# Kernel tuning notes

Measured on AMD Instinct MI355X. Metric: run time of the kernel, lower is better.

## Reference

```python
import jax, jax.numpy as jnp
import numpy as np

N, K, F_IN, F_OUT, P = 50000, 32, 64, 64, 3


def setup_inputs() -> dict:
    key = jax.random.key(0)
    k1, k2, k3, k4, k5 = jax.random.split(key, 5)
    h = jax.random.normal(k1, (N, F_IN), dtype=jnp.float32)
    pos = jax.random.normal(k2, (N, P), dtype=jnp.float32)
    neighbor_idx = jax.random.randint(k3, (N, K), 0, N, dtype=jnp.int32)
    weight = jax.random.normal(k4, (K * F_IN, F_OUT), dtype=jnp.float32) * 0.02
    bias_p = jax.random.normal(k5, (1, F_OUT), dtype=jnp.float32) * 0.02
    return {"h": h, "pos": pos, "neighbor_idx": neighbor_idx,
            "weight": weight, "bias_p": bias_p}


def reference(h, pos, neighbor_idx, weight, bias_p):
    n, k = neighbor_idx.shape
    msgs = h[neighbor_idx]                      # [N, K, F_IN] gather
    diff = pos[:, None, :] - pos[neighbor_idx]  # [N, K, P]
    sq = jnp.sum(diff * diff, axis=2, keepdims=True)  # [N, K, 1]
    # torch: dist[dist==0] = 0.5 ; safe-sqrt avoids NaN grads at 0
    dist = jnp.where(sq == 0.0, 0.5, jnp.sqrt(jnp.where(sq == 0.0, 1.0, sq)))
    wow = (msgs / dist).reshape(n, k * h.shape[1])  # [N, K*F_IN]
    h1 = wow @ weight + bias_p                   # [N, F_OUT]
    return jax.nn.leaky_relu(h1, negative_slope=0.01)
```

## Files before the change

### kernel.cpp

```cpp
#include <hip/hip_runtime.h>


#define N_NODES 50000
#define KN      32
#define FIN     64
#define FOUT    64
#define MTILE   64

typedef __attribute__((ext_vector_type(4))) float    f32x4;
typedef __attribute__((ext_vector_type(8))) _Float16 f16x8;

static __device__ __forceinline__ f16x8 dec8i(unsigned int x, unsigned int y) {
    union { unsigned int w[4]; f16x8 v; } r;
    unsigned int xh = x >> 16, yh = y >> 16;
    r.w[0] = 0x64006400u | ((x  & 0xFFu) << 2) | ((x  & 0xFF00u) << 10);
    r.w[1] = 0x64006400u | ((xh & 0xFFu) << 2) | ((xh & 0xFF00u) << 10);
    r.w[2] = 0x64006400u | ((y  & 0xFFu) << 2) | ((y  & 0xFF00u) << 10);
    r.w[3] = 0x64006400u | ((yh & 0xFFu) << 2) | ((yh & 0xFF00u) << 10);
    return r.v;
}

__global__ void k_prep(const float* __restrict__ w, _Float16* __restrict__ wf,
                       const float* __restrict__ h, unsigned char* __restrict__ hq,
                       const float* __restrict__ pos, float4* __restrict__ posx) {
    __shared__ float s_w[64 * 64];
    const int tid = threadIdx.x;
    if (blockIdx.x < 32) {
        const int kn = blockIdx.x;
        for (int p = tid; p < 64 * 64; p += 256)
            s_w[p] = w[kn * 64 * 64 + p];
        __syncthreads();
        const int t = tid >> 6, lane = tid & 63;
        const int lm = lane & 15, q = lane >> 4;
        #pragma unroll
        for (int jh = 0; jh < 2; ++jh) {
            f16x8 o;
            #pragma unroll
            for (int i = 0; i < 8; ++i)
                o[i] = (_Float16)s_w[(q * 16 + jh * 8 + i) * 64 + t * 16 + lm];
            *(f16x8*)(wf + ((kn * 2 + jh) * 4 + t) * 512 + lane * 8) = o;
        }
    } else {
        const int r = (blockIdx.x - 32) * 256 + tid;
        if (r < N_NODES) {
            const float* hr = h + (size_t)r * FIN;
            float v[64];
            float amax = 0.f;
            #pragma unroll
            for (int i = 0; i < 16; ++i) {
                float4 t4 = ((const float4*)hr)[i];
                v[i * 4 + 0] = t4.x; v[i * 4 + 1] = t4.y;
                v[i * 4 + 2] = t4.z; v[i * 4 + 3] = t4.w;
                amax = fmaxf(amax, fmaxf(fmaxf(fabsf(t4.x), fabsf(t4.y)),
                                         fmaxf(fabsf(t4.z), fabsf(t4.w))));
            }
            float scale = fmaxf(amax, 1e-30f) * (1.0f / 126.0f);
            float inv = 126.0f / fmaxf(amax, 1e-30f);
            union { unsigned char c[64]; uint4 u4[4]; } o;
            #pragma unroll
            for (int i = 0; i < 64; ++i) {
                int q8 = __float2int_rn(v[i] * inv);
                o.c[i] = (unsigned char)(q8 + 128);
            }
            uint4* dst = (uint4*)(hq + (size_t)r * 64);
            dst[0] = o.u4[0]; dst[1] = o.u4[1]; dst[2] = o.u4[2]; dst[3] = o.u4[3];
            float4 px;
            px.x = pos[r * 3 + 0]; px.y = pos[r * 3 + 1]; px.z = pos[r * 3 + 2];
            px.w = scale;
            posx[r] = px;
        }
    }
}

__global__ __launch_bounds__(256, 4) void k_main(
        const unsigned char* __restrict__ hq,
        const float4*        __restrict__ posx,
        const int*           __restrict__ nidx,
        const _Float16*      __restrict__ wf,
        const float*         __restrict__ bias,
        float*               __restrict__ out)
{
    __shared__ __align__(16) char smem[2 * 64 * 68 * 4];
    int2*  s_e   = (int2*)smem;
    float* s_red = (float*)smem;

    const int tid = threadIdx.x;
    const int m0  = blockIdx.x * MTILE;

    for (int p = tid; p < MTILE * KN; p += 256) {
        int m = p & 63, k = p >> 6;
        int node = m0 + m;
        int idx = 0; float c1 = 0.f;
        if (node < N_NODES) {
            idx = nidx[node * KN + k];
            float4 pn = posx[node];
            float4 pi = posx[idx];
            float dx = pn.x - pi.x, dy = pn.y - pi.y, dz = pn.z - pi.z;
            float sq = dx * dx + dy * dy + dz * dz;
            float scl = (sq == 0.f) ? 2.0f : rsqrtf(sq);
            c1 = pi.w * scl * 0.25f;
        }
        s_e[k * MTILE + m] = make_int2(idx, __float_as_int(c1));
    }
    __syncthreads();

    const int lane = tid & 63, kg = tid >> 6;
    const int lm = lane & 15, q = lane >> 4;

    const _Float16* pb = wf + lane * 8;

    f32x4 acc[4][4] = {};

    #pragma unroll 1
    for (int j = 0; j < 8; ++j) {
        const int kn = kg * 8 + j;
        int2 e0 = s_e[kn * MTILE + lm];
        int2 e1 = s_e[kn * MTILE + 16 + lm];
        int2 e2 = s_e[kn * MTILE + 32 + lm];
        int2 e3 = s_e[kn * MTILE + 48 + lm];
        uint4 d0 = *(const uint4*)(hq + (size_t)e0.x * 64 + q * 16);
        uint4 d1 = *(const uint4*)(hq + (size_t)e1.x * 64 + q * 16);
        uint4 d2 = *(const uint4*)(hq + (size_t)e2.x * 64 + q * 16);
        uint4 d3 = *(const uint4*)(hq + (size_t)e3.x * 64 + q * 16);
        const _Float16 c0 = (_Float16)__int_as_float(e0.y);
        const _Float16 c1 = (_Float16)__int_as_float(e1.y);
        const _Float16 c2 = (_Float16)__int_as_float(e2.y);
        const _Float16 c3 = (_Float16)__int_as_float(e3.y);
        const _Float16 K = (_Float16)1536.0f;

        {
            const _Float16* pbb = pb + (kn * 2 + 0) * 2048;
            f16x8 b0 = *(const f16x8*)(pbb);
            f16x8 b1 = *(const f16x8*)(pbb + 512);
            f16x8 b2 = *(const f16x8*)(pbb + 1024);
            f16x8 b3 = *(const f16x8*)(pbb + 1536);
            f16x8 a0 = (dec8i(d0.x, d0.y) - K) * c0;
            f16x8 a1 = (dec8i(d1.x, d1.y) - K) * c1;
            f16x8 a2 = (dec8i(d2.x, d2.y) - K) * c2;
            f16x8 a3 = (dec8i(d3.x, d3.y) - K) * c3;
            acc[0][0] = __builtin_amdgcn_mfma_f32_16x16x32_f16(a0, b0, acc[0][0], 0, 0, 0);
            acc[0][1] = __builtin_amdgcn_mfma_f32_16x16x32_f16(a0, b1, acc[0][1], 0, 0, 0);
            acc[0][2] = __builtin_amdgcn_mfma_f32_16x16x32_f16(a0, b2, acc[0][2], 0, 0, 0);
            acc[0][3] = __builtin_amdgcn_mfma_f32_16x16x32_f16(a0, b3, acc[0][3], 0, 0, 0);
            acc[1][0] = __builtin_amdgcn_mfma_f32_16x16x32_f16(a1, b0, acc[1][0], 0, 0, 0);
            acc[1][1] = __builtin_amdgcn_mfma_f32_16x16x32_f16(a1, b1, acc[1][1], 0, 0, 0);
            acc[1][2] = __builtin_amdgcn_mfma_f32_16x16x32_f16(a1, b2, acc[1][2], 0, 0, 0);
            acc[1][3] = __builtin_amdgcn_mfma_f32_16x16x32_f16(a1, b3, acc[1][3], 0, 0, 0);
            acc[2][0] = __builtin_amdgcn_mfma_f32_16x16x32_f16(a2, b0, acc[2][0], 0, 0, 0);
            acc[2][1] = __builtin_amdgcn_mfma_f32_16x16x32_f16(a2, b1, acc[2][1], 0, 0, 0);
            acc[2][2] = __builtin_amdgcn_mfma_f32_16x16x32_f16(a2, b2, acc[2][2], 0, 0, 0);
            acc[2][3] = __builtin_amdgcn_mfma_f32_16x16x32_f16(a2, b3, acc[2][3], 0, 0, 0);
            acc[3][0] = __builtin_amdgcn_mfma_f32_16x16x32_f16(a3, b0, acc[3][0], 0, 0, 0);
            acc[3][1] = __builtin_amdgcn_mfma_f32_16x16x32_f16(a3, b1, acc[3][1], 0, 0, 0);
            acc[3][2] = __builtin_amdgcn_mfma_f32_16x16x32_f16(a3, b2, acc[3][2], 0, 0, 0);
            acc[3][3] = __builtin_amdgcn_mfma_f32_16x16x32_f16(a3, b3, acc[3][3], 0, 0, 0);
        }
        {
            const _Float16* pbb = pb + (kn * 2 + 1) * 2048;
            f16x8 b0 = *(const f16x8*)(pbb);
            f16x8 b1 = *(const f16x8*)(pbb + 512);
            f16x8 b2 = *(const f16x8*)(pbb + 1024);
            f16x8 b3 = *(const f16x8*)(pbb + 1536);
            f16x8 a0 = (dec8i(d0.z, d0.w) - K) * c0;
            f16x8 a1 = (dec8i(d1.z, d1.w) - K) * c1;
            f16x8 a2 = (dec8i(d2.z, d2.w) - K) * c2;
            f16x8 a3 = (dec8i(d3.z, d3.w) - K) * c3;
            acc[0][0] = __builtin_amdgcn_mfma_f32_16x16x32_f16(a0, b0, acc[0][0], 0, 0, 0);
            acc[0][1] = __builtin_amdgcn_mfma_f32_16x16x32_f16(a0, b1, acc[0][1], 0, 0, 0);
            acc[0][2] = __builtin_amdgcn_mfma_f32_16x16x32_f16(a0, b2, acc[0][2], 0, 0, 0);
            acc[0][3] = __builtin_amdgcn_mfma_f32_16x16x32_f16(a0, b3, acc[0][3], 0, 0, 0);
            acc[1][0] = __builtin_amdgcn_mfma_f32_16x16x32_f16(a1, b0, acc[1][0], 0, 0, 0);
            acc[1][1] = __builtin_amdgcn_mfma_f32_16x16x32_f16(a1, b1, acc[1][1], 0, 0, 0);
            acc[1][2] = __builtin_amdgcn_mfma_f32_16x16x32_f16(a1, b2, acc[1][2], 0, 0, 0);
            acc[1][3] = __builtin_amdgcn_mfma_f32_16x16x32_f16(a1, b3, acc[1][3], 0, 0, 0);
            acc[2][0] = __builtin_amdgcn_mfma_f32_16x16x32_f16(a2, b0, acc[2][0], 0, 0, 0);
            acc[2][1] = __builtin_amdgcn_mfma_f32_16x16x32_f16(a2, b1, acc[2][1], 0, 0, 0);
            acc[2][2] = __builtin_amdgcn_mfma_f32_16x16x32_f16(a2, b2, acc[2][2], 0, 0, 0);
            acc[2][3] = __builtin_amdgcn_mfma_f32_16x16x32_f16(a2, b3, acc[2][3], 0, 0, 0);
            acc[3][0] = __builtin_amdgcn_mfma_f32_16x16x32_f16(a3, b0, acc[3][0], 0, 0, 0);
            acc[3][1] = __builtin_amdgcn_mfma_f32_16x16x32_f16(a3, b1, acc[3][1], 0, 0, 0);
            acc[3][2] = __builtin_amdgcn_mfma_f32_16x16x32_f16(a3, b2, acc[3][2], 0, 0, 0);
            acc[3][3] = __builtin_amdgcn_mfma_f32_16x16x32_f16(a3, b3, acc[3][3], 0, 0, 0);
        }
    }

    __syncthreads();

    float* reg = s_red + (kg & 1) * (64 * 68);
    if (kg < 2) {
        #pragma unroll
        for (int mt = 0; mt < 4; ++mt)
            #pragma unroll
            for (int t = 0; t < 4; ++t)
                #pragma unroll
                for (int r = 0; r < 4; ++r)
                    reg[(mt * 16 + q * 4 + r) * 68 + t * 16 + lm] = acc[mt][t][r];
    }
    __syncthreads();
    if (kg >= 2) {
        #pragma unroll
        for (int mt = 0; mt < 4; ++mt)
            #pragma unroll
            for (int t = 0; t < 4; ++t)
                #pragma unroll
                for (int r = 0; r < 4; ++r)
                    reg[(mt * 16 + q * 4 + r) * 68 + t * 16 + lm] += acc[mt][t][r];
    }
    __syncthreads();

    const int row = tid >> 2, c0e = (tid & 3) * 16;
    const int node = m0 + row;
    if (node < N_NODES) {
        #pragma unroll
        for (int i = 0; i < 4; ++i) {
            int c = c0e + i * 4;
            f32x4 v0 = *(const f32x4*)(s_red + row * 68 + c);
            f32x4 v1 = *(const f32x4*)(s_red + 64 * 68 + row * 68 + c);
            f32x4 bb = *(const f32x4*)(bias + c);
            f32x4 o = v0 + v1 + bb;
            #pragma unroll
            for (int jj = 0; jj < 4; ++jj) o[jj] = o[jj] > 0.f ? o[jj] : 0.01f * o[jj];
            *(f32x4*)(out + node * FOUT + c) = o;
        }
    }
}

extern "C" void kernel_launch(void* const* d_in, const int* in_sizes, int n_in,
                              void* d_out, int out_size, void* d_ws, size_t ws_size,
                              hipStream_t stream) {
    const float* h    = (const float*)d_in[0];
    const float* pos  = (const float*)d_in[1];
    const int*   nidx = (const int*)d_in[2];
    const float* w    = (const float*)d_in[3];
    const float* bias = (const float*)d_in[4];
    float* out = (float*)d_out;

    _Float16*      wf   = (_Float16*)d_ws;
    unsigned char* hq   = (unsigned char*)d_ws + 262144;
    float4*        posx = (float4*)((char*)d_ws + 262144 + 3200000);

    const int h_blocks = (N_NODES + 255) / 256;
    k_prep<<<32 + h_blocks, 256, 0, stream>>>(w, wf, h, hq, pos, posx);
    k_main<<<(N_NODES + MTILE - 1) / MTILE, 256, 0, stream>>>(hq, posx, nidx, wf, bias, out);
}
```

Baseline: 115.5 us.

## Quantize weights to int8 per-column and split h quantization across four threads

Weights are now stored as uint8 with a per-output-column fp16 scale and decoded to fp16 inside the main loop, halving the weight bytes each wave loads per step. The prep kernel also quantizes each h row with four threads using shuffle-based max reduction instead of one thread per row, which raises parallelism and coalescing. The cost is extra ALU decode work per MFMA step in the hot loop and additional weight quantization error.

```diff
diff --git a/kernel.cpp b/kernel.cpp
--- a/kernel.cpp
+++ b/kernel.cpp
@@ -20,54 +20,73 @@
     return r.v;
 }
 
-__global__ void k_prep(const float* __restrict__ w, _Float16* __restrict__ wf,
+__global__ void k_prep(const float* __restrict__ w, unsigned char* __restrict__ wq,
+                       _Float16* __restrict__ wsc,
                        const float* __restrict__ h, unsigned char* __restrict__ hq,
                        const float* __restrict__ pos, float4* __restrict__ posx) {
     __shared__ float s_w[64 * 64];
+    __shared__ float s_scale[64];
     const int tid = threadIdx.x;
     if (blockIdx.x < 32) {
         const int kn = blockIdx.x;
         for (int p = tid; p < 64 * 64; p += 256)
             s_w[p] = w[kn * 64 * 64 + p];
         __syncthreads();
+        if (tid < 64) {
+            float amax = 0.f;
+            for (int r = 0; r < 64; ++r)
+                amax = fmaxf(amax, fabsf(s_w[r * 64 + tid]));
+            float s = fmaxf(amax, 1e-30f) * (1.0f / 126.0f);
+            s_scale[tid] = s;
+            wsc[kn * 64 + tid] = (_Float16)(s * 0.25f);
+        }
+        __syncthreads();
         const int t = tid >> 6, lane = tid & 63;
         const int lm = lane & 15, q = lane >> 4;
+        const float inv = 1.0f / s_scale[t * 16 + lm];
         #pragma unroll
         for (int jh = 0; jh < 2; ++jh) {
-            f16x8 o;
-            #pragma unroll
-            for (int i = 0; i < 8; ++i)
-                o[i] = (_Float16)s_w[(q * 16 + jh * 8 + i) * 64 + t * 16 + lm];
-            *(f16x8*)(wf + ((kn * 2 + jh) * 4 + t) * 512 + lane * 8) = o;
+            union { unsigned char c[8]; uint2 u; } o;
+            #pragma unroll
+            for (int i = 0; i < 8; ++i) {
+                float wv = s_w[(q * 16 + jh * 8 + i) * 64 + t * 16 + lm];
+                int q8 = __float2int_rn(wv * inv);
+                o.c[i] = (unsigned char)(q8 + 128);
+            }
+            *(uint2*)(wq + (size_t)((kn * 2 + jh) * 4 + t) * 512 + lane * 8) = o.u;
         }
     } else {
-        const int r = (blockIdx.x - 32) * 256 + tid;
+        const int r   = (blockIdx.x - 32) * 64 + (tid >> 2);
+        const int sub = tid & 3;
         if (r < N_NODES) {
-            const float* hr = h + (size_t)r * FIN;
-            float v[64];
+            const float* hr = h + (size_t)r * FIN + sub * 16;
+            float v[16];
             float amax = 0.f;
             #pragma unroll
-            for (int i = 0; i < 16; ++i) {
+            for (int i = 0; i < 4; ++i) {
                 float4 t4 = ((const float4*)hr)[i];
                 v[i * 4 + 0] = t4.x; v[i * 4 + 1] = t4.y;
                 v[i * 4 + 2] = t4.z; v[i * 4 + 3] = t4.w;
                 amax = fmaxf(amax, fmaxf(fmaxf(fabsf(t4.x), fabsf(t4.y)),
                                          fmaxf(fabsf(t4.z), fabsf(t4.w))));
             }
+            amax = fmaxf(amax, __shfl_xor(amax, 1));
+            amax = fmaxf(amax, __shfl_xor(amax, 2));
             float scale = fmaxf(amax, 1e-30f) * (1.0f / 126.0f);
-            float inv = 126.0f / fmaxf(amax, 1e-30f);
-            union { unsigned char c[64]; uint4 u4[4]; } o;
-            #pragma unroll
-            for (int i = 0; i < 64; ++i) {
+            float inv   = 126.0f / fmaxf(amax, 1e-30f);
+            union { unsigned char c[16]; uint4 u4; } o;
+            #pragma unroll
+            for (int i = 0; i < 16; ++i) {
                 int q8 = __float2int_rn(v[i] * inv);
                 o.c[i] = (unsigned char)(q8 + 128);
             }
-            uint4* dst = (uint4*)(hq + (size_t)r * 64);
-            dst[0] = o.u4[0]; dst[1] = o.u4[1]; dst[2] = o.u4[2]; dst[3] = o.u4[3];
-            float4 px;
-            px.x = pos[r * 3 + 0]; px.y = pos[r * 3 + 1]; px.z = pos[r * 3 + 2];
-            px.w = scale;
-            posx[r] = px;
+            *(uint4*)(hq + (size_t)r * 64 + sub * 16) = o.u4;
+            if (sub == 0) {
+                float4 px;
+                px.x = pos[r * 3 + 0]; px.y = pos[r * 3 + 1]; px.z = pos[r * 3 + 2];
+                px.w = scale;
+                posx[r] = px;
+            }
         }
     }
 }
@@ -76,7 +95,8 @@
         const unsigned char* __restrict__ hq,
         const float4*        __restrict__ posx,
         const int*           __restrict__ nidx,
-        const _Float16*      __restrict__ wf,
+        const unsigned char* __restrict__ wq,
+        const _Float16*      __restrict__ wsc,
         const float*         __restrict__ bias,
         float*               __restrict__ out)
 {
@@ -106,8 +126,6 @@
 
     const int lane = tid & 63, kg = tid >> 6;
     const int lm = lane & 15, q = lane >> 4;
-
-    const _Float16* pb = wf + lane * 8;
 
     f32x4 acc[4][4] = {};
 
@@ -126,14 +144,23 @@
         const _Float16 c1 = (_Float16)__int_as_float(e1.y);
         const _Float16 c2 = (_Float16)__int_as_float(e2.y);
         const _Float16 c3 = (_Float16)__int_as_float(e3.y);
+        const _Float16* wsk = wsc + kn * 64;
+        const _Float16 sb0 = wsk[lm];
+        const _Float16 sb1 = wsk[16 + lm];
+        const _Float16 sb2 = wsk[32 + lm];
+        const _Float16 sb3 = wsk[48 + lm];
         const _Float16 K = (_Float16)1536.0f;
 
         {
-            const _Float16* pbb = pb + (kn * 2 + 0) * 2048;
-            f16x8 b0 = *(const f16x8*)(pbb);
-            f16x8 b1 = *(const f16x8*)(pbb + 512);
-            f16x8 b2 = *(const f16x8*)(pbb + 1024);
-            f16x8 b3 = *(const f16x8*)(pbb + 1536);
+            const unsigned char* pq = wq + (size_t)((kn * 2 + 0) * 4) * 512 + lane * 8;
+            uint2 w0 = *(const uint2*)(pq);
+            uint2 w1 = *(const uint2*)(pq + 512);
+            uint2 w2 = *(const uint2*)(pq + 1024);
+            uint2 w3 = *(const uint2*)(pq + 1536);
+            f16x8 b0 = (dec8i(w0.x, w0.y) - K) * sb0;
+            f16x8 b1 = (dec8i(w1.x, w1.y) - K) * sb1;
+            f16x8 b2 = (dec8i(w2.x, w2.y) - K) * sb2;
+            f16x8 b3 = (dec8i(w3.x, w3.y) - K) * sb3;
             f16x8 a0 = (dec8i(d0.x, d0.y) - K) * c0;
             f16x8 a1 = (dec8i(d1.x, d1.y) - K) * c1;
             f16x8 a2 = (dec8i(d2.x, d2.y) - K) * c2;
@@ -156,11 +183,15 @@
             acc[3][3] = __builtin_amdgcn_mfma_f32_16x16x32_f16(a3, b3, acc[3][3], 0, 0, 0);
         }
         {
-            const _Float16* pbb = pb + (kn * 2 + 1) * 2048;
-            f16x8 b0 = *(const f16x8*)(pbb);
-            f16x8 b1 = *(const f16x8*)(pbb + 512);
-            f16x8 b2 = *(const f16x8*)(pbb + 1024);
-            f16x8 b3 = *(const f16x8*)(pbb + 1536);
+            const unsigned char* pq = wq + (size_t)((kn * 2 + 1) * 4) * 512 + lane * 8;
+            uint2 w0 = *(const uint2*)(pq);
+            uint2 w1 = *(const uint2*)(pq + 512);
+            uint2 w2 = *(const uint2*)(pq + 1024);
+            uint2 w3 = *(const uint2*)(pq + 1536);
+            f16x8 b0 = (dec8i(w0.x, w0.y) - K) * sb0;
+            f16x8 b1 = (dec8i(w1.x, w1.y) - K) * sb1;
+            f16x8 b2 = (dec8i(w2.x, w2.y) - K) * sb2;
+            f16x8 b3 = (dec8i(w3.x, w3.y) - K) * sb3;
             f16x8 a0 = (dec8i(d0.z, d0.w) - K) * c0;
             f16x8 a1 = (dec8i(d1.z, d1.w) - K) * c1;
             f16x8 a2 = (dec8i(d2.z, d2.w) - K) * c2;
@@ -235,11 +266,12 @@
     const float* bias = (const float*)d_in[4];
     float* out = (float*)d_out;
 
-    _Float16*      wf   = (_Float16*)d_ws;
+    unsigned char* wq   = (unsigned char*)d_ws;
+    _Float16*      wsc  = (_Float16*)((char*)d_ws + 131072);
     unsigned char* hq   = (unsigned char*)d_ws + 262144;
     float4*        posx = (float4*)((char*)d_ws + 262144 + 3200000);
 
-    const int h_blocks = (N_NODES + 255) / 256;
-    k_prep<<<32 + h_blocks, 256, 0, stream>>>(w, wf, h, hq, pos, posx);
-    k_main<<<(N_NODES + MTILE - 1) / MTILE, 256, 0, stream>>>(hq, posx, nidx, wf, bias, out);
-}
+    const int h_blocks = (N_NODES + 63) / 64;
+    k_prep<<<32 + h_blocks, 256, 0, stream>>>(w, wq, wsc, h, hq, pos, posx);
+    k_main<<<(N_NODES + MTILE - 1) / MTILE, 256, 0, stream>>>(hq, posx, nidx, wq, wsc, bias, out);
+}
```

Result: slower. 125.8 us (+8.9%).
